# Performance work log

Hardware: AMD Instinct MI355X
Metric: run time of the kernel (lower is better)

## Reference

```python
import jax, jax.numpy as jnp
import numpy as np
from jax import lax

H_IMG, W_IMG = 1280, 1280
STRIDES = (8, 16, 32, 64, 128)
FEAT_SHAPES = tuple((H_IMG // s) * (W_IMG // s) for s in STRIDES)  # (25600,6400,1600,400,100)
N_POINTS = sum(FEAT_SHAPES)  # 34100
NUM_CLASSES = 1
TOPK = 1000
SCORE_THRESH = 0.05
NMS_THRESH = 0.5
MAX_DET = 300
BATCH = 8
N_GT = 200


def make_points():
    # matches AnchorFreePS.reference_points: cell centers at stride*i + stride//2, (cx, cy) order
    pts = []
    for s in STRIDES:
        h, w = H_IMG // s, W_IMG // s
        cx = np.arange(w, dtype=np.float32) * s + s // 2
        cy = np.arange(h, dtype=np.float32) * s + s // 2
        gy, gx = np.meshgrid(cy, cx, indexing='ij')
        pts.append(np.stack([gx, gy], axis=-1).reshape(-1, 2))
    return jnp.asarray(np.concatenate(pts, axis=0))


def setup_inputs() -> dict:
    key = jax.random.key(0)
    k1, k2, k3, k4 = jax.random.split(key, 4)
    points = make_points()  # [N,2]
    xy = jax.random.uniform(k1, (BATCH, N_GT, 2), minval=0.0, maxval=1000.0)
    wh = jax.random.uniform(k2, (BATCH, N_GT, 2), minval=20.0, maxval=260.0)
    gt_boxes = jnp.concatenate([xy, xy + wh], axis=-1)  # [B,M,4] x1y1x2y2
    cls_logits = jax.random.normal(k3, (BATCH, N_POINTS, NUM_CLASSES)) * 1.5 - 3.0
    regression = jax.random.uniform(k4, (BATCH, N_POINTS, 4)) * 0.1  # normalized ltrb codes
    return {"points": points, "gt_boxes": gt_boxes, "cls_logits": cls_logits, "regression": regression}


def match_points_to_boxes(points, gt_boxes):
    # point-in-box test + area-cost argmin (compute_loss matched_idxs)
    px = points[None, :, None, 0]  # [1,N,1]
    py = points[None, :, None, 1]
    b = gt_boxes[:, None, :, :]    # [B,1,M,4]
    inside = (px >= b[..., 0]) & (px <= b[..., 2]) & (py >= b[..., 1]) & (py <= b[..., 3])  # [B,N,M]
    matched = jnp.any(inside, axis=-1)  # [B,N]
    areas = (gt_boxes[..., 2] - gt_boxes[..., 0]) * (gt_boxes[..., 3] - gt_boxes[..., 1])  # [B,M]
    BIG = jnp.float32(2 ** 31 - 1)  # torch.iinfo(torch.int).max
    cost = jnp.where(inside, areas[:, None, :], BIG)
    idx = jnp.argmin(cost, axis=-1)
    return jnp.where(matched, idx, -1)


def decode_boxes(rel, pts):
    # FCOSBoxCoder.decode_single with weights (1,1,1,1)
    l = rel[:, 0] * W_IMG
    t = rel[:, 1] * H_IMG
    r = rel[:, 2] * W_IMG
    b = rel[:, 3] * H_IMG
    x, y = pts[:, 0], pts[:, 1]
    return jnp.stack([x - l, y - t, x + r, y + b], axis=-1)


def clip_boxes(boxes):
    return jnp.stack([
        jnp.clip(boxes[:, 0], 0.0, W_IMG),
        jnp.clip(boxes[:, 1], 0.0, H_IMG),
        jnp.clip(boxes[:, 2], 0.0, W_IMG),
        jnp.clip(boxes[:, 3], 0.0, H_IMG)], axis=-1)


def nms(boxes, scores, labels, valid_init):
    # fixed-size sequential NMS equivalent to batched_nms (same-label suppression)
    work = lax.stop_gradient(jnp.where(valid_init, scores, -jnp.inf))

    def body(w, _):
        i = jnp.argmax(w)
        s = w[i]
        box = boxes[i]
        x1 = jnp.maximum(box[0], boxes[:, 0])
        y1 = jnp.maximum(box[1], boxes[:, 1])
        x2 = jnp.minimum(box[2], boxes[:, 2])
        y2 = jnp.minimum(box[3], boxes[:, 3])
        inter = jnp.clip(x2 - x1, 0.0) * jnp.clip(y2 - y1, 0.0)
        a1 = (box[2] - box[0]) * (box[3] - box[1])
        a2 = (boxes[:, 2] - boxes[:, 0]) * (boxes[:, 3] - boxes[:, 1])
        iou = inter / (a1 + a2 - inter + 1e-9)
        supp = (iou > NMS_THRESH) & (labels == labels[i])
        w = jnp.where(supp, -jnp.inf, w).at[i].set(-jnp.inf)
        return w, (i, s)

    _, (idxs, picked) = lax.scan(body, work, None, length=MAX_DET)
    valid = picked > -jnp.inf
    return idxs, valid


def postprocess_image(points, cls_i, reg_i):
    bx_list, sc_list, lb_list = [], [], []
    off = 0
    for size in FEAT_SHAPES:  # fixed small level loop
        sl = slice(off, off + size)
        off += size
        scores = jax.nn.sigmoid(cls_i[sl]).reshape(-1)  # [size*C]
        k = min(TOPK, size * NUM_CLASSES)
        sc, idx = lax.top_k(scores, k)
        a = idx // NUM_CLASSES
        lb = idx % NUM_CLASSES
        bx = clip_boxes(decode_boxes(reg_i[sl][a], points[sl][a]))
        bx_list.append(bx)
        sc_list.append(sc)
        lb_list.append(lb)
    boxes = jnp.concatenate(bx_list, axis=0)
    scores = jnp.concatenate(sc_list, axis=0)
    labels = jnp.concatenate(lb_list, axis=0)
    idxs, valid = nms(boxes, scores, labels, scores > SCORE_THRESH)
    out_boxes = jnp.where(valid[:, None], boxes[idxs], 0.0)
    out_scores = jnp.where(valid, scores[idxs], 0.0)
    out_labels = jnp.where(valid, labels[idxs], -1)
    return out_boxes, out_scores, out_labels, valid


def reference(points, gt_boxes, cls_logits, regression):
    matched_idxs = match_points_to_boxes(points, gt_boxes)  # [B,N]
    boxes, scores, labels, valid = jax.vmap(
        lambda c, r: postprocess_image(points, c, r))(cls_logits, regression)
    return matched_idxs, boxes, scores, labels, valid
```

## Files before the change

### kernel.cpp

```cpp
#include <hip/hip_runtime.h>
#include <stdint.h>

#define N_POINTS   34100
#define BATCH      8
#define N_GT       200
#define NLEV       5
#define NCAND      3500
#define MAX_DET    300
#define SCORE_TH   0.05f
#define NMS_TH     0.5f
#define IMG        1280.0f
#define TIE_CAP    2048
#define NBIN       4096
#define MTH 0.50000002980232238769531250

#define OUT_MATCH  0
#define OUT_BOXES  272800
#define OUT_SCORES 282400
#define OUT_LABELS 284800
#define OUT_VALID  287200

#define WS_KEYS    0
#define WS_SBOX    2632192
#define WS_SSC     3080192
#define WS_MASK    3192192
#define WS_DIAG    9500032
#define MASK_STRIDE 98560
#define DIAG_STRIDE 3520

typedef unsigned long long u64;
typedef uint32_t u32;

__device__ __forceinline__ int mask_off(int c) {
    int g = c >> 6;
    return 64 * (55 * g - (g * (g - 1)) / 2) + (c - (g << 6)) * (55 - g);
}

__device__ __forceinline__ int loff_of(int l) {
    return (l == 0) ? 0 : (l == 1) ? 25600 : (l == 2) ? 32000 : (l == 3) ? 33600 : 34000;
}
__device__ __forceinline__ int lsize_of(int l) {
    return (l == 0) ? 25600 : (l == 1) ? 6400 : (l == 2) ? 1600 : (l == 3) ? 400 : 100;
}
__device__ __forceinline__ int k_of(int l) {
    return (l == 0) ? 1000 : (l == 1) ? 1000 : (l == 2) ? 1000 : (l == 3) ? 400 : 100;
}
__device__ __forceinline__ u64 readlane64(u64 v, int t) {
    u32 lo = (u32)__builtin_amdgcn_readlane((int)(u32)v, t);
    u32 hi = (u32)__builtin_amdgcn_readlane((int)(u32)(v >> 32), t);
    return ((u64)hi << 32) | lo;
}

#define MPT 2
__global__ __launch_bounds__(256)
void match_key_kernel(const float* __restrict__ points,
                      const float* __restrict__ gt,
                      const float* __restrict__ logits,
                      float* __restrict__ out_match,
                      u32* __restrict__ keys) {
#pragma clang fp contract(off)
    __shared__ float bx1[N_GT], by1[N_GT], bx2[N_GT], by2[N_GT], ar[N_GT];
    const int b = blockIdx.y;
    const int base = blockIdx.x * (256 * MPT) + threadIdx.x;

    for (int j = threadIdx.x; j < N_GT; j += 256) {
        float x1 = gt[(b * N_GT + j) * 4 + 0];
        float y1 = gt[(b * N_GT + j) * 4 + 1];
        float x2 = gt[(b * N_GT + j) * 4 + 2];
        float y2 = gt[(b * N_GT + j) * 4 + 3];
        bx1[j] = x1; by1[j] = y1; bx2[j] = x2; by2[j] = y2;
        ar[j] = (x2 - x1) * (y2 - y1);
    }
    __syncthreads();

    const float BIGF = 2147483648.0f;
    float px[MPT], py[MPT], best[MPT];
    int bi[MPT];
#pragma unroll
    for (int k = 0; k < MPT; ++k) {
        int p = base + k * 256;
        int pc = (p < N_POINTS) ? p : 0;
        px[k] = points[pc * 2 + 0];
        py[k] = points[pc * 2 + 1];
        best[k] = BIGF; bi[k] = -1;
    }
    for (int j = 0; j < N_GT; ++j) {
        float x1 = bx1[j], y1 = by1[j], x2 = bx2[j], y2 = by2[j], a = ar[j];
#pragma unroll
        for (int k = 0; k < MPT; ++k) {
            bool inside = (px[k] >= x1) && (px[k] <= x2) &&
                          (py[k] >= y1) && (py[k] <= y2);
            float cost = inside ? a : BIGF;
            if (cost < best[k]) { best[k] = cost; bi[k] = j; }
        }
    }
#pragma unroll
    for (int k = 0; k < MPT; ++k) {
        int p = base + k * 256;
        if (p >= N_POINTS) continue;
        out_match[b * N_POINTS + p] = (float)bi[k];
        float lg = logits[b * N_POINTS + p];
        float s = 1.0f / (1.0f + expf(-lg));
        u32 u = __float_as_uint(s);
        u32 key = (u & 0x80000000u) ? ~u : (u | 0x80000000u);
        keys[b * N_POINTS + p] = key;
    }
}

#define SORT_T 1024
__global__ __launch_bounds__(SORT_T)
void pipeline_kernel(const u32* __restrict__ keys,
                     const float* __restrict__ reg,
                     const float* __restrict__ points,
                     float* __restrict__ sboxes,
                     float* __restrict__ sscores) {
#pragma clang fp contract(off)
    __shared__ u64 sk[4096];
    __shared__ u64 aux[4096];
    __shared__ u64 tb[TIE_CAP];
    __shared__ u32 h[4096];
    __shared__ u32 bs[4096];
    __shared__ u32 wt[16];
    __shared__ u32 sT, skk, scnt, stcnt, stb;
    const int b = blockIdx.x;
    const int tid = threadIdx.x;
    const int lane = tid & 63;

    if (tid == 0) scnt = 0u;

    for (int l = 0; l < NLEV; ++l) {
        const int n = lsize_of(l);
        const u32 K = (u32)k_of(l);
        const u32* kl = keys + b * N_POINTS + loff_of(l);

        for (int i = tid; i < NBIN; i += SORT_T) h[i] = 0u;
        if (tid == 0) stcnt = 0u;
        __syncthreads();
        for (int i = tid; i < n; i += SORT_T)
            atomicAdd(&h[(kl[i] >> 19) & 4095u], 1u);
        __syncthreads();

        if (tid < 64) {
            u32 S = 0;
#pragma unroll 8
            for (int i = 0; i < 64; ++i) S += h[lane * 64 + i];
            u32 acc = S;
#pragma unroll
            for (int off = 1; off < 64; off <<= 1) {
                u32 v = (u32)__shfl_down((int)acc, off);
                if (lane + off < 64) acc += v;
            }
            u32 sfxAfter = acc - S;
            bool hit = (sfxAfter < K) && (sfxAfter + S >= K);
            u64 bal = __ballot(hit);
            int Lg = (int)__builtin_ctzll(bal);
            u32 sfxG = (u32)__shfl((int)sfxAfter, Lg);

            u32 v = h[Lg * 64 + lane];
            u32 acc2 = v;
#pragma unroll
            for (int off = 1; off < 64; off <<= 1) {
                u32 t = (u32)__shfl_down((int)acc2, off);
                if (lane + off < 64) acc2 += t;
            }
            u32 sfx2 = sfxG + acc2 - v;
            bool hit2 = (sfx2 < K) && (sfx2 + v >= K);
            if (hit2) { sT = (u32)(Lg * 64 + lane); skk = K - sfx2; }
        }
        __syncthreads();
        const u32 T = sT;
        const u64 below = (lane == 0) ? 0ull : (~0ull >> (64 - lane));

        for (int i0 = tid; i0 - tid < n; i0 += SORT_T) {
            bool active = i0 < n;
            u32 key = active ? kl[i0] : 0u;
            u32 digit = (key >> 19) & 4095u;
            bool isDef = active && (digit > T);
            bool isTie = active && (digit == T);
            u64 k50 = ((u64)key << 18) | ((u64)(7 - l) << 15)
                    | (u64)(32767 - i0);
            u64 grp = __ballot(isDef);
            if (grp) {
                int leader = (int)__builtin_ctzll(grp);
                u32 base_ = 0;
                if (lane == leader)
                    base_ = atomicAdd(&scnt, (u32)__builtin_popcountll(grp));
                base_ = (u32)__shfl((int)base_, leader);
                if (isDef)
                    sk[base_ + (u32)__builtin_popcountll(grp & below)] = k50;
            }
            u64 tg = __ballot(isTie);
            if (tg) {
                int leader = (int)__builtin_ctzll(tg);
                u32 base_ = 0;
                if (lane == leader)
                    base_ = atomicAdd(&stcnt, (u32)__builtin_popcountll(tg));
                base_ = (u32)__shfl((int)base_, leader);
                if (isTie) {
                    u32 pos = base_ + (u32)__builtin_popcountll(tg & below);
                    if (pos < TIE_CAP) tb[pos] = k50;
                }
            }
        }
        __syncthreads();
        int t = (int)stcnt; if (t > TIE_CAP) t = TIE_CAP;
        const int kk = (int)skk;
        if (tid == 0) stb = atomicAdd(&scnt, (u32)kk);
        __syncthreads();
        const int tbase = (int)stb;
        for (int j = tid; j < t; j += SORT_T) {
            u64 kj = tb[j];
            int r = 0;
            for (int i = 0; i < t; ++i) r += (tb[i] > kj) ? 1 : 0;
            if (r < kk) sk[tbase + r] = kj;
        }
        __syncthreads();
    }
    const int total = (int)scnt;

    for (int i = tid; i < 4096; i += SORT_T) h[i] = 0u;
    __syncthreads();
    for (int i = tid; i < total; i += SORT_T)
        atomicAdd(&h[(u32)(sk[i] >> 37) & 4095u], 1u);
    __syncthreads();

    u32 t0 = h[4095 - 4 * tid];
    u32 t1 = h[4095 - (4 * tid + 1)];
    u32 t2 = h[4095 - (4 * tid + 2)];
    u32 t3 = h[4095 - (4 * tid + 3)];
    u32 tsum = t0 + t1 + t2 + t3;
    u32 sc_ = tsum;
#pragma unroll
    for (int off = 1; off < 64; off <<= 1) {
        u32 v = (u32)__shfl_up((int)sc_, off);
        if (lane >= off) sc_ += v;
    }
    if (lane == 63) wt[tid >> 6] = sc_;
    __syncthreads();
    if (tid < 64) {
        u32 v = (tid < 16) ? wt[tid] : 0u;
        u32 s2 = v;
#pragma unroll
        for (int off = 1; off < 16; off <<= 1) {
            u32 x = (u32)__shfl_up((int)s2, off);
            if (tid >= off) s2 += x;
        }
        if (tid < 16) wt[tid] = s2 - v;
    }
    __syncthreads();
    u32 run = (sc_ - tsum) + wt[tid >> 6];
    bs[4095 - 4 * tid] = run;       run += t0;
    bs[4095 - (4 * tid + 1)] = run; run += t1;
    bs[4095 - (4 * tid + 2)] = run; run += t2;
    bs[4095 - (4 * tid + 3)] = run;
    __syncthreads();
    for (int i = tid; i < 4096; i += SORT_T) h[i] = 0u;
    __syncthreads();
    for (int i = tid; i < total; i += SORT_T) {
        u64 k = sk[i];
        u32 d = (u32)(k >> 37) & 4095u;
        u32 pos = bs[d] + atomicAdd(&h[d], 1u);
        aux[pos] = k;
    }
    __syncthreads();
    for (int p = tid; p < total; p += SORT_T) {
        u64 kp = aux[p];
        u32 d = (u32)(kp >> 37) & 4095u;
        u32 gbase = bs[d];
        u32 gend = (d == 0) ? (u32)total : bs[d - 1];
        u32 r = 0;
        for (u32 q = gbase; q < gend; ++q) r += (aux[q] > kp) ? 1u : 0u;
        sk[gbase + r] = kp;
    }
    __syncthreads();

    for (int r = tid; r < NCAND; r += SORT_T) {
        float x1 = 0.f, y1 = 0.f, x2 = 0.f, y2 = 0.f, sc = 0.f;
        if (r < total) {
            u64 k50 = sk[r];
            int lowb = (int)(k50 & 0x3FFFFull);
            int l = 7 - (lowb >> 15);
            int idxl = 32767 - (lowb & 32767);
            int p = loff_of(l) + idxl;
            u32 key32 = (u32)(k50 >> 18);
            sc = __uint_as_float(key32 ^ 0x80000000u);
            int gp = b * N_POINTS + p;
            float l_ = reg[gp * 4 + 0] * IMG;
            float t_ = reg[gp * 4 + 1] * IMG;
            float r_ = reg[gp * 4 + 2] * IMG;
            float bb = reg[gp * 4 + 3] * IMG;
            float px = points[p * 2 + 0];
            float py = points[p * 2 + 1];
            x1 = fminf(fmaxf(px - l_, 0.0f), IMG);
            y1 = fminf(fmaxf(py - t_, 0.0f), IMG);
            x2 = fminf(fmaxf(px + r_, 0.0f), IMG);
            y2 = fminf(fmaxf(py + bb, 0.0f), IMG);
        }
        int slot = b * NCAND + r;
        sboxes[slot * 4 + 0] = x1;
        sboxes[slot * 4 + 1] = y1;
        sboxes[slot * 4 + 2] = x2;
        sboxes[slot * 4 + 3] = y2;
        sscores[slot] = sc;
    }
}

__global__ __launch_bounds__(256)
void mask_kernel(const float* __restrict__ sboxes,
                 const float* __restrict__ sscores,
                 u64* __restrict__ mask,
                 u64* __restrict__ diag) {
#pragma clang fp contract(off)
    const int b = blockIdx.y;
    const int wv = threadIdx.x >> 6;
    const int lane = threadIdx.x & 63;
    const int NG = (NCAND + 3) >> 2;
    const int gidx = blockIdx.x * 4 + wv;
    if (gidx >= NG) return;
    const int c0 = gidx << 2;

    const float4* gb = (const float4*)sboxes + b * NCAND;
    const float* gs = sscores + b * NCAND;
    u64* mout = mask + (size_t)b * MASK_STRIDE;
    u64* dout = diag + (size_t)b * DIAG_STRIDE;

    float4 bc[4]; float a1[4]; bool ok[4]; int g[4]; u64* rp[4];
    bool any = false;
#pragma unroll
    for (int i = 0; i < 4; ++i) {
        int c = c0 + i;
        int cc = (c < NCAND) ? c : (NCAND - 1);
        bc[i] = gb[cc];
        a1[i] = (bc[i].z - bc[i].x) * (bc[i].w - bc[i].y);
        ok[i] = (c < NCAND) && (gs[cc] > SCORE_TH);
        g[i] = cc >> 6;
        rp[i] = mout + mask_off(cc) - g[i];
        any |= ok[i];
    }
    if (!any) return;

    for (int w = (c0 >> 6); w < 55; ++w) {
        int cj = (w << 6) + lane;
        float4 bj = (cj < NCAND) ? gb[cj] : make_float4(0.f, 0.f, 0.f, 0.f);
        float a2 = (bj.z - bj.x) * (bj.w - bj.y);
#pragma unroll
        for (int i = 0; i < 4; ++i) {
            float x1 = fmaxf(bc[i].x, bj.x);
            float y1 = fmaxf(bc[i].y, bj.y);
            float x2 = fminf(bc[i].z, bj.z);
            float y2 = fminf(bc[i].w, bj.w);
            float inter = fmaxf(x2 - x1, 0.f) * fmaxf(y2 - y1, 0.f);
            float denom = a1[i] + a2 - inter + 1e-9f;
            float hf = 0.5f * denom;
            float rr = fmaf(0x1p-25f, denom, hf);
            u64 bits = __ballot(inter > rr);
            u64 eq = __ballot(inter == rr);
            if (eq) {
                u64 fb = __ballot((double)inter > MTH * (double)denom);
                bits |= (eq & fb);
            }
            if (lane == 0 && ok[i] && w >= g[i]) {
                rp[i][w] = bits;
                if (w == g[i]) dout[c0 + i] = bits;
            }
        }
    }
}

__global__ __launch_bounds__(64)
void scan_kernel(const float* __restrict__ sboxes,
                 const float* __restrict__ sscores,
                 const u64* __restrict__ mask,
                 const u64* __restrict__ diag,
                 float* __restrict__ out) {
    const int b = blockIdx.x;
    const int lane = threadIdx.x;
    const float4* gb = (const float4*)sboxes + b * NCAND;
    const float* gs = sscores + b * NCAND;
    const u64* mrow = mask + (size_t)b * MASK_STRIDE;
    const u64* drow = diag + (size_t)b * DIAG_STRIDE;

    float* ob = out + OUT_BOXES  + b * MAX_DET * 4;
    float* os = out + OUT_SCORES + b * MAX_DET;
    float* ol = out + OUT_LABELS + b * MAX_DET;
    float* ov = out + OUT_VALID  + b * MAX_DET;

    u64 m = 0ull;
    u64 rowN = drow[lane];
    float4 bjN = gb[lane];
    float sjN = gs[lane];

    int kept = 0;
    for (int w = 0; w < 55; ++w) {
        const int wbase = w << 6;
        const u64 row = rowN;
        const float4 bj = bjN;
        const float sj = sjN;
        if (w < 54) {
            int cn = wbase + 64 + lane;
            int cc = (cn < NCAND) ? cn : (NCAND - 1);
            rowN = drow[cc];
            bjN = gb[cc];
            float s = gs[cc];
            sjN = (cn < NCAND) ? s : 0.f;
        }
        int c = wbase + lane;
        u64 bad = __ballot(!((c < NCAND) && (sj > SCORE_TH)));
        u64 cur = readlane64(m, w) | bad;
        u64 km = 0ull;
        while (kept < MAX_DET) {
            u64 avail = ~cur;
            if (avail == 0ull) break;
            int t = (int)__builtin_ctzll(avail);
            u64 r = readlane64(row, t);
            cur |= r | (1ull << t);
            km |= 1ull << t;
            if (lane == t) {
                ob[kept * 4 + 0] = bj.x;
                ob[kept * 4 + 1] = bj.y;
                ob[kept * 4 + 2] = bj.z;
                ob[kept * 4 + 3] = bj.w;
                os[kept] = sj;
                ol[kept] = 0.0f;
                ov[kept] = 1.0f;
            }
            kept++;
        }
        if (km) {
            const bool lr = (lane >= w && lane < 55);
            const int lo = lane - w;
            u64 acc = 0ull;
            while (km) {
#define POPBIT(tn) int tn = -1; if (km) { tn = (int)__builtin_ctzll(km); km &= km - 1ull; }
                POPBIT(t0) POPBIT(t1) POPBIT(t2) POPBIT(t3)
                POPBIT(t4) POPBIT(t5) POPBIT(t6) POPBIT(t7)
#undef POPBIT
                u64 v0 = 0, v1 = 0, v2 = 0, v3 = 0, v4 = 0, v5 = 0, v6 = 0, v7 = 0;
                if (lr) {
                    v0 = mrow[mask_off(wbase + t0) + lo];
                    if (t1 >= 0) v1 = mrow[mask_off(wbase + t1) + lo];
                    if (t2 >= 0) v2 = mrow[mask_off(wbase + t2) + lo];
                    if (t3 >= 0) v3 = mrow[mask_off(wbase + t3) + lo];
                    if (t4 >= 0) v4 = mrow[mask_off(wbase + t4) + lo];
                    if (t5 >= 0) v5 = mrow[mask_off(wbase + t5) + lo];
                    if (t6 >= 0) v6 = mrow[mask_off(wbase + t6) + lo];
                    if (t7 >= 0) v7 = mrow[mask_off(wbase + t7) + lo];
                }
                acc |= ((v0 | v1) | (v2 | v3)) | ((v4 | v5) | (v6 | v7));
            }
            m |= acc;
        }
        if (kept >= MAX_DET) break;
    }
    for (int k = kept + lane; k < MAX_DET; k += 64) {
        ob[k * 4 + 0] = 0.f; ob[k * 4 + 1] = 0.f;
        ob[k * 4 + 2] = 0.f; ob[k * 4 + 3] = 0.f;
        os[k] = 0.f; ol[k] = -1.f; ov[k] = 0.f;
    }
}

extern "C" void kernel_launch(void* const* d_in, const int* in_sizes, int n_in,
                              void* d_out, int out_size, void* d_ws, size_t ws_size,
                              hipStream_t stream) {
    const float* points = (const float*)d_in[0];
    const float* gt     = (const float*)d_in[1];
    const float* logits = (const float*)d_in[2];
    const float* reg    = (const float*)d_in[3];
    float* out = (float*)d_out;

    u32* keys   = (u32*)((char*)d_ws + WS_KEYS);
    float* sboxes  = (float*)((char*)d_ws + WS_SBOX);
    float* sscores = (float*)((char*)d_ws + WS_SSC);
    u64* mask   = (u64*)((char*)d_ws + WS_MASK);
    u64* diag   = (u64*)((char*)d_ws + WS_DIAG);

    dim3 g1((N_POINTS + 256 * MPT - 1) / (256 * MPT), BATCH);
    match_key_kernel<<<g1, 256, 0, stream>>>(points, gt, logits,
                                             out + OUT_MATCH, keys);

    pipeline_kernel<<<BATCH, SORT_T, 0, stream>>>(keys, reg, points,
                                                  sboxes, sscores);

    dim3 g5(((NCAND + 3) / 4 + 3) / 4, BATCH);
    mask_kernel<<<g5, 256, 0, stream>>>(sboxes, sscores, mask, diag);

    scan_kernel<<<BATCH, 64, 0, stream>>>(sboxes, sscores, mask, diag, out);
}
```

Before: 276.7 us.

## Fuse sigmoid key computation into pipeline and batch all levels in one pass

Result: no change. 279.9 us (+1.2%).

```diff
diff --git a/kernel.cpp b/kernel.cpp
--- a/kernel.cpp
+++ b/kernel.cpp
@@ -10,8 +10,8 @@
 #define SCORE_TH   0.05f
 #define NMS_TH     0.5f
 #define IMG        1280.0f
-#define TIE_CAP    2048
 #define NBIN       4096
+#define TIE_CAP    4096
 #define MTH 0.50000002980232238769531250
 
 #define OUT_MATCH  0
@@ -20,7 +20,6 @@
 #define OUT_LABELS 284800
 #define OUT_VALID  287200
 
-#define WS_KEYS    0
 #define WS_SBOX    2632192
 #define WS_SSC     3080192
 #define WS_MASK    3192192
@@ -36,11 +35,11 @@
     return 64 * (55 * g - (g * (g - 1)) / 2) + (c - (g << 6)) * (55 - g);
 }
 
+__device__ __forceinline__ int level_of(int p) {
+    return (p < 25600) ? 0 : (p < 32000) ? 1 : (p < 33600) ? 2 : (p < 34000) ? 3 : 4;
+}
 __device__ __forceinline__ int loff_of(int l) {
     return (l == 0) ? 0 : (l == 1) ? 25600 : (l == 2) ? 32000 : (l == 3) ? 33600 : 34000;
-}
-__device__ __forceinline__ int lsize_of(int l) {
-    return (l == 0) ? 25600 : (l == 1) ? 6400 : (l == 2) ? 1600 : (l == 3) ? 400 : 100;
 }
 __device__ __forceinline__ int k_of(int l) {
     return (l == 0) ? 1000 : (l == 1) ? 1000 : (l == 2) ? 1000 : (l == 3) ? 400 : 100;
@@ -50,14 +49,17 @@
     u32 hi = (u32)__builtin_amdgcn_readlane((int)(u32)(v >> 32), t);
     return ((u64)hi << 32) | lo;
 }
+__device__ __forceinline__ u32 sigkey(float lg) {
+    float s = 1.0f / (1.0f + expf(-lg));
+    u32 u = __float_as_uint(s);
+    return (u & 0x80000000u) ? ~u : (u | 0x80000000u);
+}
 
 #define MPT 2
 __global__ __launch_bounds__(256)
-void match_key_kernel(const float* __restrict__ points,
-                      const float* __restrict__ gt,
-                      const float* __restrict__ logits,
-                      float* __restrict__ out_match,
-                      u32* __restrict__ keys) {
+void match_kernel(const float* __restrict__ points,
+                  const float* __restrict__ gt,
+                  float* __restrict__ out_match) {
 #pragma clang fp contract(off)
     __shared__ float bx1[N_GT], by1[N_GT], bx2[N_GT], by2[N_GT], ar[N_GT];
     const int b = blockIdx.y;
@@ -97,128 +99,135 @@
 #pragma unroll
     for (int k = 0; k < MPT; ++k) {
         int p = base + k * 256;
-        if (p >= N_POINTS) continue;
-        out_match[b * N_POINTS + p] = (float)bi[k];
-        float lg = logits[b * N_POINTS + p];
-        float s = 1.0f / (1.0f + expf(-lg));
-        u32 u = __float_as_uint(s);
-        u32 key = (u & 0x80000000u) ? ~u : (u | 0x80000000u);
-        keys[b * N_POINTS + p] = key;
+        if (p < N_POINTS) out_match[b * N_POINTS + p] = (float)bi[k];
     }
 }
 
 #define SORT_T 1024
 __global__ __launch_bounds__(SORT_T)
-void pipeline_kernel(const u32* __restrict__ keys,
+void pipeline_kernel(const float* __restrict__ logits,
                      const float* __restrict__ reg,
                      const float* __restrict__ points,
                      float* __restrict__ sboxes,
                      float* __restrict__ sscores) {
 #pragma clang fp contract(off)
-    __shared__ u64 sk[4096];
-    __shared__ u64 aux[4096];
-    __shared__ u64 tb[TIE_CAP];
-    __shared__ u32 h[4096];
-    __shared__ u32 bs[4096];
-    __shared__ u32 wt[16];
-    __shared__ u32 sT, skk, scnt, stcnt, stb;
+    __shared__ __align__(16) char smem[131072];
+    u64* sk   = (u64*)smem;
+    u32* hist = (u32*)(smem + 32768);
+    u64* tb   = (u64*)(smem + 32768);
+    u64* aux  = (u64*)(smem + 65536);
+    u32* h    = (u32*)(smem + 98304);
+    u32* bs   = (u32*)(smem + 114688);
+    __shared__ u32 sTl[NLEV], skkl[NLEV], wt[16];
+    __shared__ u32 scnt, stcnt;
+
     const int b = blockIdx.x;
     const int tid = threadIdx.x;
     const int lane = tid & 63;
-
-    if (tid == 0) scnt = 0u;
-
-    for (int l = 0; l < NLEV; ++l) {
-        const int n = lsize_of(l);
-        const u32 K = (u32)k_of(l);
-        const u32* kl = keys + b * N_POINTS + loff_of(l);
-
-        for (int i = tid; i < NBIN; i += SORT_T) h[i] = 0u;
-        if (tid == 0) stcnt = 0u;
-        __syncthreads();
-        for (int i = tid; i < n; i += SORT_T)
-            atomicAdd(&h[(kl[i] >> 19) & 4095u], 1u);
-        __syncthreads();
-
-        if (tid < 64) {
-            u32 S = 0;
+    const int wid = tid >> 6;
+    const float* lg = logits + b * N_POINTS;
+
+    for (int i = tid; i < NLEV * NBIN; i += SORT_T) hist[i] = 0u;
+    if (tid == 0) { scnt = 0u; stcnt = 0u; }
+    __syncthreads();
+    for (int i = tid; i < N_POINTS; i += SORT_T) {
+        u32 key = sigkey(lg[i]);
+        atomicAdd(&hist[level_of(i) * NBIN + ((key >> 19) & 4095u)], 1u);
+    }
+    __syncthreads();
+
+    if (wid < NLEV) {
+        const u32 K = (u32)k_of(wid);
+        const u32* hh = hist + wid * NBIN;
+        u32 S = 0;
 #pragma unroll 8
-            for (int i = 0; i < 64; ++i) S += h[lane * 64 + i];
-            u32 acc = S;
-#pragma unroll
-            for (int off = 1; off < 64; off <<= 1) {
-                u32 v = (u32)__shfl_down((int)acc, off);
-                if (lane + off < 64) acc += v;
+        for (int i = 0; i < 64; ++i) S += hh[lane * 64 + i];
+        u32 acc = S;
+#pragma unroll
+        for (int off = 1; off < 64; off <<= 1) {
+            u32 v = (u32)__shfl_down((int)acc, off);
+            if (lane + off < 64) acc += v;
+        }
+        u32 sfxAfter = acc - S;
+        bool hit = (sfxAfter < K) && (sfxAfter + S >= K);
+        u64 bal = __ballot(hit);
+        int Lg = (int)__builtin_ctzll(bal);
+        u32 sfxG = (u32)__shfl((int)sfxAfter, Lg);
+
+        u32 v = hh[Lg * 64 + lane];
+        u32 acc2 = v;
+#pragma unroll
+        for (int off = 1; off < 64; off <<= 1) {
+            u32 t = (u32)__shfl_down((int)acc2, off);
+            if (lane + off < 64) acc2 += t;
+        }
+        u32 sfx2 = sfxG + acc2 - v;
+        bool hit2 = (sfx2 < K) && (sfx2 + v >= K);
+        if (hit2) { sTl[wid] = (u32)(Lg * 64 + lane); skkl[wid] = K - sfx2; }
+    }
+    __syncthreads();
+
+    const u64 below = (lane == 0) ? 0ull : (~0ull >> (64 - lane));
+    for (int i0 = tid; i0 - tid < N_POINTS; i0 += SORT_T) {
+        bool active = i0 < N_POINTS;
+        int pc = active ? i0 : (N_POINTS - 1);
+        u32 key = sigkey(lg[pc]);
+        int l = level_of(pc);
+        u32 digit = (key >> 19) & 4095u;
+        u32 T = sTl[l];
+        bool isDef = active && (digit > T);
+        bool isTie = active && (digit == T);
+        u64 k50 = ((u64)key << 18) | ((u64)(7 - l) << 15)
+                | (u64)(32767 - (pc - loff_of(l)));
+        u64 grp = __ballot(isDef);
+        if (grp) {
+            int leader = (int)__builtin_ctzll(grp);
+            u32 base_ = 0;
+            if (lane == leader)
+                base_ = atomicAdd(&scnt, (u32)__builtin_popcountll(grp));
+            base_ = (u32)__shfl((int)base_, leader);
+            if (isDef) sk[base_ + (u32)__builtin_popcountll(grp & below)] = k50;
+        }
+        u64 tg = __ballot(isTie);
+        if (tg) {
+            int leader = (int)__builtin_ctzll(tg);
+            u32 base_ = 0;
+            if (lane == leader)
+                base_ = atomicAdd(&stcnt, (u32)__builtin_popcountll(tg));
+            base_ = (u32)__shfl((int)base_, leader);
+            if (isTie) {
+                u32 pos = base_ + (u32)__builtin_popcountll(tg & below);
+                if (pos < TIE_CAP) tb[pos] = k50;
             }
-            u32 sfxAfter = acc - S;
-            bool hit = (sfxAfter < K) && (sfxAfter + S >= K);
-            u64 bal = __ballot(hit);
-            int Lg = (int)__builtin_ctzll(bal);
-            u32 sfxG = (u32)__shfl((int)sfxAfter, Lg);
-
-            u32 v = h[Lg * 64 + lane];
-            u32 acc2 = v;
-#pragma unroll
-            for (int off = 1; off < 64; off <<= 1) {
-                u32 t = (u32)__shfl_down((int)acc2, off);
-                if (lane + off < 64) acc2 += t;
-            }
-            u32 sfx2 = sfxG + acc2 - v;
-            bool hit2 = (sfx2 < K) && (sfx2 + v >= K);
-            if (hit2) { sT = (u32)(Lg * 64 + lane); skk = K - sfx2; }
-        }
-        __syncthreads();
-        const u32 T = sT;
-        const u64 below = (lane == 0) ? 0ull : (~0ull >> (64 - lane));
-
-        for (int i0 = tid; i0 - tid < n; i0 += SORT_T) {
-            bool active = i0 < n;
-            u32 key = active ? kl[i0] : 0u;
-            u32 digit = (key >> 19) & 4095u;
-            bool isDef = active && (digit > T);
-            bool isTie = active && (digit == T);
-            u64 k50 = ((u64)key << 18) | ((u64)(7 - l) << 15)
-                    | (u64)(32767 - i0);
-            u64 grp = __ballot(isDef);
-            if (grp) {
-                int leader = (int)__builtin_ctzll(grp);
-                u32 base_ = 0;
-                if (lane == leader)
-                    base_ = atomicAdd(&scnt, (u32)__builtin_popcountll(grp));
-                base_ = (u32)__shfl((int)base_, leader);
-                if (isDef)
-                    sk[base_ + (u32)__builtin_popcountll(grp & below)] = k50;
-            }
-            u64 tg = __ballot(isTie);
-            if (tg) {
-                int leader = (int)__builtin_ctzll(tg);
-                u32 base_ = 0;
-                if (lane == leader)
-                    base_ = atomicAdd(&stcnt, (u32)__builtin_popcountll(tg));
-                base_ = (u32)__shfl((int)base_, leader);
-                if (isTie) {
-                    u32 pos = base_ + (u32)__builtin_popcountll(tg & below);
-                    if (pos < TIE_CAP) tb[pos] = k50;
-                }
-            }
-        }
-        __syncthreads();
-        int t = (int)stcnt; if (t > TIE_CAP) t = TIE_CAP;
-        const int kk = (int)skk;
-        if (tid == 0) stb = atomicAdd(&scnt, (u32)kk);
-        __syncthreads();
-        const int tbase = (int)stb;
-        for (int j = tid; j < t; j += SORT_T) {
-            u64 kj = tb[j];
-            int r = 0;
-            for (int i = 0; i < t; ++i) r += (tb[i] > kj) ? 1 : 0;
-            if (r < kk) sk[tbase + r] = kj;
-        }
-        __syncthreads();
-    }
+        }
+    }
+    __syncthreads();
+
+    int t = (int)stcnt; if (t > TIE_CAP) t = TIE_CAP;
+    for (int j0 = tid; j0 - tid < t; j0 += SORT_T) {
+        bool active = j0 < t;
+        u64 kj = active ? tb[j0] : 0ull;
+        u32 lvtag = (u32)(kj >> 15) & 7u;
+        int r = 0;
+        for (int i = 0; i < t; ++i) {
+            u64 ki = tb[i];
+            r += (ki > kj && (((u32)(ki >> 15) & 7u) == lvtag)) ? 1 : 0;
+        }
+        bool inc = active && (r < (int)skkl[7 - lvtag]);
+        u64 grp = __ballot(inc);
+        if (grp) {
+            int leader = (int)__builtin_ctzll(grp);
+            u32 base_ = 0;
+            if (lane == leader)
+                base_ = atomicAdd(&scnt, (u32)__builtin_popcountll(grp));
+            base_ = (u32)__shfl((int)base_, leader);
+            if (inc) sk[base_ + (u32)__builtin_popcountll(grp & below)] = kj;
+        }
+    }
+    __syncthreads();
     const int total = (int)scnt;
 
-    for (int i = tid; i < 4096; i += SORT_T) h[i] = 0u;
+    for (int i = tid; i < NBIN; i += SORT_T) h[i] = 0u;
     __syncthreads();
     for (int i = tid; i < total; i += SORT_T)
         atomicAdd(&h[(u32)(sk[i] >> 37) & 4095u], 1u);
@@ -235,7 +244,7 @@
         u32 v = (u32)__shfl_up((int)sc_, off);
         if (lane >= off) sc_ += v;
     }
-    if (lane == 63) wt[tid >> 6] = sc_;
+    if (lane == 63) wt[wid] = sc_;
     __syncthreads();
     if (tid < 64) {
         u32 v = (tid < 16) ? wt[tid] : 0u;
@@ -248,13 +257,13 @@
         if (tid < 16) wt[tid] = s2 - v;
     }
     __syncthreads();
-    u32 run = (sc_ - tsum) + wt[tid >> 6];
+    u32 run = (sc_ - tsum) + wt[wid];
     bs[4095 - 4 * tid] = run;       run += t0;
     bs[4095 - (4 * tid + 1)] = run; run += t1;
     bs[4095 - (4 * tid + 2)] = run; run += t2;
     bs[4095 - (4 * tid + 3)] = run;
     __syncthreads();
-    for (int i = tid; i < 4096; i += SORT_T) h[i] = 0u;
+    for (int i = tid; i < NBIN; i += SORT_T) h[i] = 0u;
     __syncthreads();
     for (int i = tid; i < total; i += SORT_T) {
         u64 k = sk[i];
@@ -468,18 +477,16 @@
     const float* reg    = (const float*)d_in[3];
     float* out = (float*)d_out;
 
-    u32* keys   = (u32*)((char*)d_ws + WS_KEYS);
     float* sboxes  = (float*)((char*)d_ws + WS_SBOX);
     float* sscores = (float*)((char*)d_ws + WS_SSC);
     u64* mask   = (u64*)((char*)d_ws + WS_MASK);
     u64* diag   = (u64*)((char*)d_ws + WS_DIAG);
 
+    pipeline_kernel<<<BATCH, SORT_T, 0, stream>>>(logits, reg, points,
+                                                  sboxes, sscores);
+
     dim3 g1((N_POINTS + 256 * MPT - 1) / (256 * MPT), BATCH);
-    match_key_kernel<<<g1, 256, 0, stream>>>(points, gt, logits,
-                                             out + OUT_MATCH, keys);
-
-    pipeline_kernel<<<BATCH, SORT_T, 0, stream>>>(keys, reg, points,
-                                                  sboxes, sscores);
+    match_kernel<<<g1, 256, 0, stream>>>(points, gt, out + OUT_MATCH);
 
     dim3 g5(((NCAND + 3) / 4 + 3) / 4, BATCH);
     mask_kernel<<<g5, 256, 0, stream>>>(sboxes, sscores, mask, diag);
```
